# Kernel optimization log

Measured on AMD Instinct MI355X. Metric: run time of the kernel, lower is better.

Reference implementation:

```python
import jax, jax.numpy as jnp
import numpy as np

EPS = 1e-5  # BatchNorm1d default eps

def _conv1d(x, w, stride, pad):
    # x: [B, Cin, L], w: [Cout, Cin, K]
    return jax.lax.conv_general_dilated(
        x, w, window_strides=(stride,), padding=[(pad, pad)],
        dimension_numbers=('NCH', 'OIH', 'NCH'))

def _bn(x, g, b, m, v):
    # eval-mode BatchNorm1d with running stats; x: [B, C, L]
    scale = g / jnp.sqrt(v + EPS)
    return x * scale[None, :, None] + (b - m * scale)[None, :, None]

def _hardtanh(x):
    return jnp.clip(x, -1.0, 1.0)

def _maxpool2(x):
    B, C, L = x.shape
    return x.reshape(B, C, L // 2, 2).max(axis=-1)


def setup_inputs() -> dict:
    key = jax.random.key(0)
    ks = jax.random.split(key, 20)
    B, L = 256, 16384
    x = jax.random.normal(ks[0], (B, 1, L), dtype=jnp.float32)
    rms = jax.random.uniform(ks[1], (B, 1), dtype=jnp.float32)
    # conv weights (fan-in scaled)
    w1 = jax.random.normal(ks[2], (16, 1, 17), dtype=jnp.float32) * (1.0 / np.sqrt(1 * 17))
    w2 = jax.random.normal(ks[3], (32, 16, 9), dtype=jnp.float32) * (1.0 / np.sqrt(16 * 9))
    w3 = jax.random.normal(ks[4], (64, 32, 5), dtype=jnp.float32) * (1.0 / np.sqrt(32 * 5))
    # batchnorm params (eval mode: gamma, beta, running mean/var)
    def bn_params(k, C):
        k1, k2, k3, k4 = jax.random.split(k, 4)
        g = 1.0 + 0.1 * jax.random.normal(k1, (C,), dtype=jnp.float32)
        b = 0.1 * jax.random.normal(k2, (C,), dtype=jnp.float32)
        m = 0.1 * jax.random.normal(k3, (C,), dtype=jnp.float32)
        v = jax.random.uniform(k4, (C,), dtype=jnp.float32, minval=0.5, maxval=1.5)
        return g, b, m, v
    g1, b1, m1, v1 = bn_params(ks[5], 16)
    g2, b2, m2, v2 = bn_params(ks[6], 32)
    g3, b3, m3, v3 = bn_params(ks[7], 64)
    fc1_w = jax.random.normal(ks[8], (32, 65), dtype=jnp.float32) * (1.0 / np.sqrt(65))
    fc1_b = jnp.zeros((32,), dtype=jnp.float32)
    fc2_w = jax.random.normal(ks[9], (2, 32), dtype=jnp.float32) * (1.0 / np.sqrt(32))
    fc2_b = jnp.zeros((2,), dtype=jnp.float32)
    return dict(x=x, rms=rms, w1=w1, g1=g1, b1=b1, m1=m1, v1=v1,
                w2=w2, g2=g2, b2=b2, m2=m2, v2=v2,
                w3=w3, g3=g3, b3=b3, m3=m3, v3=v3,
                fc1_w=fc1_w, fc1_b=fc1_b, fc2_w=fc2_w, fc2_b=fc2_b)


def reference(x, rms, w1, g1, b1, m1, v1, w2, g2, b2, m2, v2,
              w3, g3, b3, m3, v3, fc1_w, fc1_b, fc2_w, fc2_b):
    # Stage 1: float conv
    h = _conv1d(x, w1, 2, 8)                 # [B,16,8192]
    h = _maxpool2(_hardtanh(_bn(h, g1, b1, m1, v1)))  # [B,16,4096]
    # Stage 2: binarized (sign) weight conv
    h = _conv1d(h, jnp.sign(w2), 2, 4)       # [B,32,2048]
    h = _maxpool2(_hardtanh(_bn(h, g2, b2, m2, v2)))  # [B,32,1024]
    # Stage 3: binarized weight conv
    h = _conv1d(h, jnp.sign(w3), 2, 2)       # [B,64,512]
    h = _maxpool2(_hardtanh(_bn(h, g3, b3, m3, v3)))  # [B,64,256]
    feat = h.mean(axis=-1)                   # AdaptiveAvgPool1d(1) -> [B,64]
    combined = jnp.concatenate([feat, rms], axis=1)   # [B,65]
    h = _hardtanh(combined @ fc1_w.T + fc1_b)
    return h @ fc2_w.T + fc2_b               # [B,2]
```

## Files before the change

### kernel.cpp

```cpp
#include <hip/hip_runtime.h>

#define EPS 1e-5f

typedef float f32x4 __attribute__((ext_vector_type(4)));
typedef short s16x8 __attribute__((ext_vector_type(8)));

union FragU { uint4 u; s16x8 s; };

__device__ __forceinline__ float ht(float x){ return fminf(fmaxf(x,-1.f),1.f); }
__device__ __forceinline__ float sgn(float v){ return (v>0.f)?1.f:((v<0.f)?-1.f:0.f); }
__device__ __forceinline__ unsigned short f2bf(float f){
    unsigned int u = __builtin_bit_cast(unsigned int, f);
    u += 0x7FFFu + ((u>>16)&1u);
    return (unsigned short)(u>>16);
}

__global__ __launch_bounds__(512) void prep(
    const float* __restrict__ w1, const float* __restrict__ w2, const float* __restrict__ w3,
    const float* g1,const float* b1,const float* m1,const float* v1,
    const float* g2,const float* b2,const float* m2,const float* v2,
    const float* g3,const float* b3,const float* m3,const float* v3,
    unsigned short* __restrict__ a1, unsigned short* __restrict__ a2,
    unsigned short* __restrict__ a3, float* __restrict__ bn){
  const int t = threadIdx.x;
  if(t < 64){
    int q = t>>4, m = t&15;
    #pragma unroll
    for(int j=0;j<8;++j){ int k = 8*q+j;
      a1[t*8+j] = f2bf((k<17)? w1[m*17+k] : 0.f); }
  }
  for(int e = t; e < 640; e += 512){
    int m = e&15, q = (e>>4)&3, hc = e>>6, c = hc%5, h = hc/5;
    int oc = m + 16*h, k = 2*c + (q>>1);
    #pragma unroll
    for(int j=0;j<8;++j){ int ic = 8*(q&1)+j;
      a2[e*8+j] = f2bf((k<9)? sgn(w2[(oc*16+ic)*9+k]) : 0.f); }
  }
  for(int e = t; e < 1280; e += 512){
    int m = e&15, q = (e>>4)&3, gc = e>>6, c = gc%5, g = gc/5;
    int oc = m + 16*g;
    #pragma unroll
    for(int j=0;j<8;++j){ int ic = 8*q+j;
      a3[e*8+j] = f2bf(sgn(w3[(oc*32+ic)*5+c])); }
  }
  if(t<16){ float s = g1[t]*rsqrtf(v1[t]+EPS); bn[t]    = s; bn[16+t]  = b1[t]-m1[t]*s; }
  if(t<32){ float s = g2[t]*rsqrtf(v2[t]+EPS); bn[32+t] = s; bn[64+t]  = b2[t]-m2[t]*s; }
  if(t<64){ float s = g3[t]*rsqrtf(v3[t]+EPS); bn[96+t] = s; bn[160+t] = b3[t]-m3[t]*s; }
}

__global__ __launch_bounds__(512, 4) void kfused(const float* __restrict__ x,
    const unsigned short* __restrict__ a1, const unsigned short* __restrict__ a2,
    const unsigned short* __restrict__ a3, const float* __restrict__ bn,
    float* __restrict__ partial){
  __shared__ __align__(16) unsigned short xs[2176];
  __shared__ __align__(16) unsigned short s1[552*24];
  __shared__ __align__(16) unsigned short s2[132*40];
  __shared__ float fws[8*32];
  const int b  = blockIdx.x >> 3;
  const int t  = blockIdx.x & 7;
  const int Q0 = 32*t;
  const int tid = threadIdx.x;
  const int lane = tid & 63, m = lane & 15, q = lane >> 4, w = tid >> 6;

  const int x0 = 64*Q0 - 56;
  const float* xrow = &x[b*16384];
  for(int i = tid; i < 544; i += 512){
    int g0 = x0 + 4*i;
    float4 v = make_float4(0.f,0.f,0.f,0.f);
    if(g0 >= 0 && g0 <= 16380) v = *(const float4*)&xrow[g0];
    uint2 pk;
    pk.x = (unsigned)f2bf(v.x) | ((unsigned)f2bf(v.y)<<16);
    pk.y = (unsigned)f2bf(v.z) | ((unsigned)f2bf(v.w)<<16);
    *(uint2*)&xs[4*i] = pk;
  }
  FragU af1; af1.u = *(const uint4*)&a1[(q*16+m)*8];
  const float4 sc1 = *(const float4*)&bn[4*q];
  const float4 sh1 = *(const float4*)&bn[16+4*q];
  __syncthreads();

  const unsigned* X32 = (const unsigned*)xs;
  for(int it = 0; it < 9; ++it){
    int tile = it*8 + w;
    if(tile < 67){
      int nl = tile*16 + m;
      int d = nl + 4*q;
      FragU bf;
      bf.u.x = X32[d]; bf.u.y = X32[d+1]; bf.u.z = X32[d+2]; bf.u.w = X32[d+3];
      f32x4 acc = {0.f,0.f,0.f,0.f};
      acc = __builtin_amdgcn_mfma_f32_16x16x32_bf16(af1.s, bf.s, acc, 0,0,0);
      float r0 = ht(acc[0]*sc1.x + sh1.x);
      float r1 = ht(acc[1]*sc1.y + sh1.y);
      float r2 = ht(acc[2]*sc1.z + sh1.z);
      float r3 = ht(acc[3]*sc1.w + sh1.w);
      float p0 = fmaxf(r0, __shfl_xor(r0,1,64));
      float p1 = fmaxf(r1, __shfl_xor(r1,1,64));
      float p2 = fmaxf(r2, __shfl_xor(r2,1,64));
      float p3 = fmaxf(r3, __shfl_xor(r3,1,64));
      if((m&1)==0){
        int ppl = nl >> 1;
        uint2 pk;
        pk.x = (unsigned)f2bf(p0) | ((unsigned)f2bf(p1)<<16);
        pk.y = (unsigned)f2bf(p2) | ((unsigned)f2bf(p3)<<16);
        *(uint2*)&s1[ppl*24 + 4*q] = pk;
      }
    }
  }
  __syncthreads();

  FragU af2[2][5];
  #pragma unroll
  for(int h=0;h<2;++h)
    #pragma unroll
    for(int c=0;c<5;++c)
      af2[h][c].u = *(const uint4*)&a2[(((h*5+c)*4+q)*16+m)*8];
  float4 sc2[2], sh2[2];
  #pragma unroll
  for(int h=0;h<2;++h){
    sc2[h] = *(const float4*)&bn[32 + 16*h + 4*q];
    sh2[h] = *(const float4*)&bn[64 + 16*h + 4*q];
  }
  for(int it = 0; it < 3; ++it){
    int tile = it*8 + w;
    if(tile < 17){
      int nl = tile*16 + m;
      f32x4 acc[2] = {{0.f,0.f,0.f,0.f},{0.f,0.f,0.f,0.f}};
      #pragma unroll
      for(int c=0;c<5;++c){
        int row = 2*nl + 2*c + (q>>1);
        FragU bf; bf.u = *(const uint4*)&s1[row*24 + 8*(q&1)];
        acc[0] = __builtin_amdgcn_mfma_f32_16x16x32_bf16(af2[0][c].s, bf.s, acc[0],0,0,0);
        acc[1] = __builtin_amdgcn_mfma_f32_16x16x32_bf16(af2[1][c].s, bf.s, acc[1],0,0,0);
      }
      #pragma unroll
      for(int h=0;h<2;++h){
        float r0 = ht(acc[h][0]*sc2[h].x + sh2[h].x);
        float r1 = ht(acc[h][1]*sc2[h].y + sh2[h].y);
        float r2 = ht(acc[h][2]*sc2[h].z + sh2[h].z);
        float r3 = ht(acc[h][3]*sc2[h].w + sh2[h].w);
        float p0 = fmaxf(r0, __shfl_xor(r0,1,64));
        float p1 = fmaxf(r1, __shfl_xor(r1,1,64));
        float p2 = fmaxf(r2, __shfl_xor(r2,1,64));
        float p3 = fmaxf(r3, __shfl_xor(r3,1,64));
        if((m&1)==0 && nl < 264){
          int ppl = nl >> 1;
          uint2 pk;
          pk.x = (unsigned)f2bf(p0) | ((unsigned)f2bf(p1)<<16);
          pk.y = (unsigned)f2bf(p2) | ((unsigned)f2bf(p3)<<16);
          *(uint2*)&s2[ppl*40 + 16*h + 4*q] = pk;
        }
      }
    }
  }
  __syncthreads();

  const int gw = w >> 2, tw = w & 3;
  FragU af3[2][5];
  #pragma unroll
  for(int gl=0;gl<2;++gl)
    #pragma unroll
    for(int c=0;c<5;++c)
      af3[gl][c].u = *(const uint4*)&a3[((((2*gw+gl)*5+c)*4+q)*16+m)*8];
  float4 sc3[2], sh3[2];
  #pragma unroll
  for(int gl=0;gl<2;++gl){
    sc3[gl] = *(const float4*)&bn[96  + 16*(2*gw+gl) + 4*q];
    sh3[gl] = *(const float4*)&bn[160 + 16*(2*gw+gl) + 4*q];
  }
  {
    int nl = tw*16 + m;
    f32x4 acc[2] = {{0.f,0.f,0.f,0.f},{0.f,0.f,0.f,0.f}};
    #pragma unroll
    for(int c=0;c<5;++c){
      int row = 2*nl + c;
      FragU bf; bf.u = *(const uint4*)&s2[row*40 + 8*q];
      acc[0] = __builtin_amdgcn_mfma_f32_16x16x32_bf16(af3[0][c].s, bf.s, acc[0],0,0,0);
      acc[1] = __builtin_amdgcn_mfma_f32_16x16x32_bf16(af3[1][c].s, bf.s, acc[1],0,0,0);
    }
    #pragma unroll
    for(int gl=0;gl<2;++gl){
      float r0 = ht(acc[gl][0]*sc3[gl].x + sh3[gl].x);
      float r1 = ht(acc[gl][1]*sc3[gl].y + sh3[gl].y);
      float r2 = ht(acc[gl][2]*sc3[gl].z + sh3[gl].z);
      float r3 = ht(acc[gl][3]*sc3[gl].w + sh3[gl].w);
      float p0 = fmaxf(r0, __shfl_xor(r0,1,64));
      float p1 = fmaxf(r1, __shfl_xor(r1,1,64));
      float p2 = fmaxf(r2, __shfl_xor(r2,1,64));
      float p3 = fmaxf(r3, __shfl_xor(r3,1,64));
      float s0 = p0, s1v = p1, s2v = p2, s3 = p3;
      s0 += __shfl_xor(s0,2,64); s0 += __shfl_xor(s0,4,64); s0 += __shfl_xor(s0,8,64);
      s1v += __shfl_xor(s1v,2,64); s1v += __shfl_xor(s1v,4,64); s1v += __shfl_xor(s1v,8,64);
      s2v += __shfl_xor(s2v,2,64); s2v += __shfl_xor(s2v,4,64); s2v += __shfl_xor(s2v,8,64);
      s3 += __shfl_xor(s3,2,64); s3 += __shfl_xor(s3,4,64); s3 += __shfl_xor(s3,8,64);
      if(m == 0)
        *(float4*)&fws[w*32 + 16*gl + 4*q] = make_float4(s0,s1v,s2v,s3);
    }
  }
  __syncthreads();
  if(tid < 64){
    int oc = tid;
    int wb = (oc >> 5) * 4;
    int ocl = oc & 31;
    float sum = fws[wb*32+ocl] + fws[(wb+1)*32+ocl] + fws[(wb+2)*32+ocl] + fws[(wb+3)*32+ocl];
    partial[(b*8 + t)*64 + oc] = sum;
  }
}

__global__ __launch_bounds__(64) void kfc(const float* __restrict__ partial,
    const float* __restrict__ rms, const float* __restrict__ fc1w,
    const float* __restrict__ fc1b, const float* __restrict__ fc2w,
    const float* __restrict__ fc2b, float* __restrict__ out){
  __shared__ float feat[64];
  __shared__ float hbuf[32];
  const int b = blockIdx.x, tid = threadIdx.x;
  float s = 0.f;
  #pragma unroll
  for(int t = 0; t < 8; ++t) s += partial[(b*8 + t)*64 + tid];
  feat[tid] = s * (1.f/256.f);
  __syncthreads();
  if(tid < 32){
    float acc = fc1b[tid];
    const float* wv = &fc1w[tid*65];
    #pragma unroll
    for(int c = 0; c < 64; ++c) acc += wv[c]*feat[c];
    acc += wv[64]*rms[b];
    hbuf[tid] = ht(acc);
  }
  __syncthreads();
  if(tid < 2){
    float acc = fc2b[tid];
    const float* wv = &fc2w[tid*32];
    #pragma unroll
    for(int j = 0; j < 32; ++j) acc += wv[j]*hbuf[j];
    out[b*2 + tid] = acc;
  }
}

extern "C" void kernel_launch(void* const* d_in, const int* in_sizes, int n_in,
                              void* d_out, int out_size, void* d_ws, size_t ws_size,
                              hipStream_t stream){
  (void)in_sizes; (void)n_in; (void)out_size; (void)ws_size;
  const float* x    = (const float*)d_in[0];
  const float* rms  = (const float*)d_in[1];
  const float* w1   = (const float*)d_in[2];
  const float* g1   = (const float*)d_in[3];
  const float* b1   = (const float*)d_in[4];
  const float* m1   = (const float*)d_in[5];
  const float* v1   = (const float*)d_in[6];
  const float* w2   = (const float*)d_in[7];
  const float* g2   = (const float*)d_in[8];
  const float* b2   = (const float*)d_in[9];
  const float* m2   = (const float*)d_in[10];
  const float* v2   = (const float*)d_in[11];
  const float* w3   = (const float*)d_in[12];
  const float* g3   = (const float*)d_in[13];
  const float* b3   = (const float*)d_in[14];
  const float* m3   = (const float*)d_in[15];
  const float* v3   = (const float*)d_in[16];
  const float* fc1w = (const float*)d_in[17];
  const float* fc1b = (const float*)d_in[18];
  const float* fc2w = (const float*)d_in[19];
  const float* fc2b = (const float*)d_in[20];
  float* out  = (float*)d_out;

  float*          partial = (float*)d_ws;
  unsigned short* a1  = (unsigned short*)(partial + 131072);
  unsigned short* a2  = a1 + 512;
  unsigned short* a3  = a2 + 5120;
  float*          bnp = (float*)(a3 + 10240);

  prep<<<1,    512, 0, stream>>>(w1, w2, w3, g1,b1,m1,v1, g2,b2,m2,v2, g3,b3,m3,v3,
                                 a1, a2, a3, bnp);
  kfused<<<2048, 512, 0, stream>>>(x, a1, a2, a3, bnp, partial);
  kfc<<<256, 64, 0, stream>>>(partial, rms, fc1w, fc1b, fc2w, fc2b, out);
}
```

Before: 141.3 us.

## Fuse FC head into conv kernel via last-block counter and use DPP reductions

The separate FC-head kernel is removed. Each of the 8 tiles per batch row now bumps an atomic counter, and the last one to finish sums the partials and computes fc1/fc2 in place, which saves a kernel launch. The lane shuffles for max-pool and the 16-lane sum now use DPP moves instead of __shfl_xor, cutting LDS permute traffic. The row sum runs over all 16 lanes and is halved to make up for the duplicated pairs. The prep kernel is split across 7 blocks and also zeroes the counters, at the cost of an extra threadfence and atomic per block.

```diff
diff --git a/kernel.cpp b/kernel.cpp
--- a/kernel.cpp
+++ b/kernel.cpp
@@ -15,52 +15,83 @@
     return (unsigned short)(u>>16);
 }
 
+#define DPP_XOR1 0xB1
+#define DPP_ROR1 0x121
+#define DPP_ROR2 0x122
+#define DPP_ROR4 0x124
+#define DPP_ROR8 0x128
+template<int C>
+__device__ __forceinline__ float dppf(float x){
+  return __builtin_bit_cast(float, __builtin_amdgcn_update_dpp(
+      0, __builtin_bit_cast(int, x), C, 0xF, 0xF, true));
+}
+__device__ __forceinline__ float poolmax(float r){ return fmaxf(r, dppf<DPP_XOR1>(r)); }
+__device__ __forceinline__ float rowsum16(float s){
+  s += dppf<DPP_ROR8>(s); s += dppf<DPP_ROR4>(s);
+  s += dppf<DPP_ROR2>(s); s += dppf<DPP_ROR1>(s);
+  return s;
+}
+
 __global__ __launch_bounds__(512) void prep(
     const float* __restrict__ w1, const float* __restrict__ w2, const float* __restrict__ w3,
     const float* g1,const float* b1,const float* m1,const float* v1,
     const float* g2,const float* b2,const float* m2,const float* v2,
     const float* g3,const float* b3,const float* m3,const float* v3,
     unsigned short* __restrict__ a1, unsigned short* __restrict__ a2,
-    unsigned short* __restrict__ a3, float* __restrict__ bn){
-  const int t = threadIdx.x;
-  if(t < 64){
-    int q = t>>4, m = t&15;
-    #pragma unroll
-    for(int j=0;j<8;++j){ int k = 8*q+j;
-      a1[t*8+j] = f2bf((k<17)? w1[m*17+k] : 0.f); }
-  }
-  for(int e = t; e < 640; e += 512){
-    int m = e&15, q = (e>>4)&3, hc = e>>6, c = hc%5, h = hc/5;
-    int oc = m + 16*h, k = 2*c + (q>>1);
-    #pragma unroll
-    for(int j=0;j<8;++j){ int ic = 8*(q&1)+j;
-      a2[e*8+j] = f2bf((k<9)? sgn(w2[(oc*16+ic)*9+k]) : 0.f); }
-  }
-  for(int e = t; e < 1280; e += 512){
-    int m = e&15, q = (e>>4)&3, gc = e>>6, c = gc%5, g = gc/5;
-    int oc = m + 16*g;
-    #pragma unroll
-    for(int j=0;j<8;++j){ int ic = 8*q+j;
-      a3[e*8+j] = f2bf(sgn(w3[(oc*32+ic)*5+c])); }
-  }
-  if(t<16){ float s = g1[t]*rsqrtf(v1[t]+EPS); bn[t]    = s; bn[16+t]  = b1[t]-m1[t]*s; }
-  if(t<32){ float s = g2[t]*rsqrtf(v2[t]+EPS); bn[32+t] = s; bn[64+t]  = b2[t]-m2[t]*s; }
-  if(t<64){ float s = g3[t]*rsqrtf(v3[t]+EPS); bn[96+t] = s; bn[160+t] = b3[t]-m3[t]*s; }
+    unsigned short* __restrict__ a3, float* __restrict__ bn, int* __restrict__ cnt){
+  const int t = threadIdx.x, bid = blockIdx.x;
+  if(bid == 0){
+    if(t < 64){
+      int q = t>>4, m = t&15;
+      #pragma unroll
+      for(int j=0;j<8;++j){ int k = 8*q+j;
+        a1[t*8+j] = f2bf((k<17)? w1[m*17+k] : 0.f); }
+    }
+    if(t<16){ float s = g1[t]*rsqrtf(v1[t]+EPS); bn[t]    = s; bn[16+t]  = b1[t]-m1[t]*s; }
+    if(t<32){ float s = g2[t]*rsqrtf(v2[t]+EPS); bn[32+t] = s; bn[64+t]  = b2[t]-m2[t]*s; }
+    if(t<64){ float s = g3[t]*rsqrtf(v3[t]+EPS); bn[96+t] = s; bn[160+t] = b3[t]-m3[t]*s; }
+  } else if(bid <= 2){
+    int e = (bid-1)*512 + t;
+    if(e < 640){
+      int m = e&15, q = (e>>4)&3, hc = e>>6, c = hc%5, h = hc/5;
+      int oc = m + 16*h, k = 2*c + (q>>1);
+      #pragma unroll
+      for(int j=0;j<8;++j){ int ic = 8*(q&1)+j;
+        a2[e*8+j] = f2bf((k<9)? sgn(w2[(oc*16+ic)*9+k]) : 0.f); }
+    }
+  } else if(bid <= 5){
+    int e = (bid-3)*512 + t;
+    if(e < 1280){
+      int m = e&15, q = (e>>4)&3, gc = e>>6, c = gc%5, g = gc/5;
+      int oc = m + 16*g;
+      #pragma unroll
+      for(int j=0;j<8;++j){ int ic = 8*q+j;
+        a3[e*8+j] = f2bf(sgn(w3[(oc*32+ic)*5+c])); }
+    }
+  } else {
+    if(t < 256) cnt[t] = 0;
+  }
 }
 
 __global__ __launch_bounds__(512, 4) void kfused(const float* __restrict__ x,
     const unsigned short* __restrict__ a1, const unsigned short* __restrict__ a2,
     const unsigned short* __restrict__ a3, const float* __restrict__ bn,
-    float* __restrict__ partial){
+    float* __restrict__ partial, int* __restrict__ cnt,
+    const float* __restrict__ rms, const float* __restrict__ fc1w,
+    const float* __restrict__ fc1b, const float* __restrict__ fc2w,
+    const float* __restrict__ fc2b, float* __restrict__ out){
   __shared__ __align__(16) unsigned short xs[2176];
   __shared__ __align__(16) unsigned short s1[552*24];
   __shared__ __align__(16) unsigned short s2[132*40];
   __shared__ float fws[8*32];
+  __shared__ float feat[64];
+  __shared__ float hbuf[32];
+  __shared__ int   lastFlag;
   const int b  = blockIdx.x >> 3;
   const int t  = blockIdx.x & 7;
   const int Q0 = 32*t;
   const int tid = threadIdx.x;
-  const int lane = tid & 63, m = lane & 15, q = lane >> 4, w = tid >> 6;
+  const int m = tid & 15, q = (tid & 63) >> 4, w = tid >> 6;
 
   const int x0 = 64*Q0 - 56;
   const float* xrow = &x[b*16384];
@@ -88,14 +119,10 @@
       bf.u.x = X32[d]; bf.u.y = X32[d+1]; bf.u.z = X32[d+2]; bf.u.w = X32[d+3];
       f32x4 acc = {0.f,0.f,0.f,0.f};
       acc = __builtin_amdgcn_mfma_f32_16x16x32_bf16(af1.s, bf.s, acc, 0,0,0);
-      float r0 = ht(acc[0]*sc1.x + sh1.x);
-      float r1 = ht(acc[1]*sc1.y + sh1.y);
-      float r2 = ht(acc[2]*sc1.z + sh1.z);
-      float r3 = ht(acc[3]*sc1.w + sh1.w);
-      float p0 = fmaxf(r0, __shfl_xor(r0,1,64));
-      float p1 = fmaxf(r1, __shfl_xor(r1,1,64));
-      float p2 = fmaxf(r2, __shfl_xor(r2,1,64));
-      float p3 = fmaxf(r3, __shfl_xor(r3,1,64));
+      float p0 = poolmax(ht(acc[0]*sc1.x + sh1.x));
+      float p1 = poolmax(ht(acc[1]*sc1.y + sh1.y));
+      float p2 = poolmax(ht(acc[2]*sc1.z + sh1.z));
+      float p3 = poolmax(ht(acc[3]*sc1.w + sh1.w));
       if((m&1)==0){
         int ppl = nl >> 1;
         uint2 pk;
@@ -133,14 +160,10 @@
       }
       #pragma unroll
       for(int h=0;h<2;++h){
-        float r0 = ht(acc[h][0]*sc2[h].x + sh2[h].x);
-        float r1 = ht(acc[h][1]*sc2[h].y + sh2[h].y);
-        float r2 = ht(acc[h][2]*sc2[h].z + sh2[h].z);
-        float r3 = ht(acc[h][3]*sc2[h].w + sh2[h].w);
-        float p0 = fmaxf(r0, __shfl_xor(r0,1,64));
-        float p1 = fmaxf(r1, __shfl_xor(r1,1,64));
-        float p2 = fmaxf(r2, __shfl_xor(r2,1,64));
-        float p3 = fmaxf(r3, __shfl_xor(r3,1,64));
+        float p0 = poolmax(ht(acc[h][0]*sc2[h].x + sh2[h].x));
+        float p1 = poolmax(ht(acc[h][1]*sc2[h].y + sh2[h].y));
+        float p2 = poolmax(ht(acc[h][2]*sc2[h].z + sh2[h].z));
+        float p3 = poolmax(ht(acc[h][3]*sc2[h].w + sh2[h].w));
         if((m&1)==0 && nl < 264){
           int ppl = nl >> 1;
           uint2 pk;
@@ -178,60 +201,54 @@
     }
     #pragma unroll
     for(int gl=0;gl<2;++gl){
-      float r0 = ht(acc[gl][0]*sc3[gl].x + sh3[gl].x);
-      float r1 = ht(acc[gl][1]*sc3[gl].y + sh3[gl].y);
-      float r2 = ht(acc[gl][2]*sc3[gl].z + sh3[gl].z);
-      float r3 = ht(acc[gl][3]*sc3[gl].w + sh3[gl].w);
-      float p0 = fmaxf(r0, __shfl_xor(r0,1,64));
-      float p1 = fmaxf(r1, __shfl_xor(r1,1,64));
-      float p2 = fmaxf(r2, __shfl_xor(r2,1,64));
-      float p3 = fmaxf(r3, __shfl_xor(r3,1,64));
-      float s0 = p0, s1v = p1, s2v = p2, s3 = p3;
-      s0 += __shfl_xor(s0,2,64); s0 += __shfl_xor(s0,4,64); s0 += __shfl_xor(s0,8,64);
-      s1v += __shfl_xor(s1v,2,64); s1v += __shfl_xor(s1v,4,64); s1v += __shfl_xor(s1v,8,64);
-      s2v += __shfl_xor(s2v,2,64); s2v += __shfl_xor(s2v,4,64); s2v += __shfl_xor(s2v,8,64);
-      s3 += __shfl_xor(s3,2,64); s3 += __shfl_xor(s3,4,64); s3 += __shfl_xor(s3,8,64);
+      float p0 = poolmax(ht(acc[gl][0]*sc3[gl].x + sh3[gl].x));
+      float p1 = poolmax(ht(acc[gl][1]*sc3[gl].y + sh3[gl].y));
+      float p2 = poolmax(ht(acc[gl][2]*sc3[gl].z + sh3[gl].z));
+      float p3 = poolmax(ht(acc[gl][3]*sc3[gl].w + sh3[gl].w));
+      float s0 = rowsum16(p0)*0.5f, s1v = rowsum16(p1)*0.5f;
+      float s2v = rowsum16(p2)*0.5f, s3 = rowsum16(p3)*0.5f;
       if(m == 0)
         *(float4*)&fws[w*32 + 16*gl + 4*q] = make_float4(s0,s1v,s2v,s3);
     }
   }
   __syncthreads();
   if(tid < 64){
-    int oc = tid;
-    int wb = (oc >> 5) * 4;
-    int ocl = oc & 31;
+    int ocl = tid & 31;
+    int wb  = (tid >> 5) * 4;
     float sum = fws[wb*32+ocl] + fws[(wb+1)*32+ocl] + fws[(wb+2)*32+ocl] + fws[(wb+3)*32+ocl];
-    partial[(b*8 + t)*64 + oc] = sum;
-  }
-}
-
-__global__ __launch_bounds__(64) void kfc(const float* __restrict__ partial,
-    const float* __restrict__ rms, const float* __restrict__ fc1w,
-    const float* __restrict__ fc1b, const float* __restrict__ fc2w,
-    const float* __restrict__ fc2b, float* __restrict__ out){
-  __shared__ float feat[64];
-  __shared__ float hbuf[32];
-  const int b = blockIdx.x, tid = threadIdx.x;
-  float s = 0.f;
-  #pragma unroll
-  for(int t = 0; t < 8; ++t) s += partial[(b*8 + t)*64 + tid];
-  feat[tid] = s * (1.f/256.f);
-  __syncthreads();
-  if(tid < 32){
-    float acc = fc1b[tid];
-    const float* wv = &fc1w[tid*65];
-    #pragma unroll
-    for(int c = 0; c < 64; ++c) acc += wv[c]*feat[c];
-    acc += wv[64]*rms[b];
-    hbuf[tid] = ht(acc);
-  }
-  __syncthreads();
-  if(tid < 2){
-    float acc = fc2b[tid];
-    const float* wv = &fc2w[tid*32];
-    #pragma unroll
-    for(int j = 0; j < 32; ++j) acc += wv[j]*hbuf[j];
-    out[b*2 + tid] = acc;
+    partial[(b*8 + t)*64 + tid] = sum;
+  }
+  if(tid == 0){
+    __threadfence();
+    int old = atomicAdd(&cnt[b], 1);
+    lastFlag = (old == 7);
+  }
+  __syncthreads();
+  if(lastFlag){
+    if(tid < 64){
+      const volatile float* pv = partial;
+      float s = 0.f;
+      #pragma unroll
+      for(int t2 = 0; t2 < 8; ++t2) s += pv[(b*8 + t2)*64 + tid];
+      feat[tid] = s * (1.f/256.f);
+    }
+    __syncthreads();
+    if(tid < 32){
+      float acc = fc1b[tid];
+      const float* wv = &fc1w[tid*65];
+      #pragma unroll
+      for(int c = 0; c < 64; ++c) acc += wv[c]*feat[c];
+      acc += wv[64]*rms[b];
+      hbuf[tid] = ht(acc);
+    }
+    __syncthreads();
+    if(tid < 2){
+      float acc = fc2b[tid];
+      const float* wv = &fc2w[tid*32];
+      #pragma unroll
+      for(int j = 0; j < 32; ++j) acc += wv[j]*hbuf[j];
+      out[b*2 + tid] = acc;
+    }
   }
 }
 
@@ -267,9 +284,10 @@
   unsigned short* a2  = a1 + 512;
   unsigned short* a3  = a2 + 5120;
   float*          bnp = (float*)(a3 + 10240);
-
-  prep<<<1,    512, 0, stream>>>(w1, w2, w3, g1,b1,m1,v1, g2,b2,m2,v2, g3,b3,m3,v3,
-                                 a1, a2, a3, bnp);
-  kfused<<<2048, 512, 0, stream>>>(x, a1, a2, a3, bnp, partial);
-  kfc<<<256, 64, 0, stream>>>(partial, rms, fc1w, fc1b, fc2w, fc2b, out);
-}
+  int*            cnt = (int*)(bnp + 224);
+
+  prep<<<7,    512, 0, stream>>>(w1, w2, w3, g1,b1,m1,v1, g2,b2,m2,v2, g3,b3,m3,v3,
+                                 a1, a2, a3, bnp, cnt);
+  kfused<<<2048, 512, 0, stream>>>(x, a1, a2, a3, bnp, partial, cnt,
+                                   rms, fc1w, fc1b, fc2w, fc2b, out);
+}
```

Measured after the change: 163.2 us. 1.15x slower.

## Halve per-block sequence tile, raise occupancy, and parallelize weight prep

Applied to the files above, without the earlier changes.

Each fused block now covers 16 pooled stage-3 outputs instead of 32. This doubles the grid to 4096 blocks, shrinks the LDS buffers, and raises launch_bounds occupancy to 8 blocks per CU. Stage-3 work is redistributed so each wave handles one 16-channel group, and halo positions outside the valid range are explicitly zeroed. The prep kernel is split across 6 blocks so weight packing runs in parallel. In exchange, the halo overhead ratio rises, since more redundant stage-1/2 work is recomputed per output, and there are twice as many partial sums to reduce.

```diff
diff --git a/kernel.cpp b/kernel.cpp
--- a/kernel.cpp
+++ b/kernel.cpp
@@ -22,49 +22,55 @@
     const float* g3,const float* b3,const float* m3,const float* v3,
     unsigned short* __restrict__ a1, unsigned short* __restrict__ a2,
     unsigned short* __restrict__ a3, float* __restrict__ bn){
-  const int t = threadIdx.x;
-  if(t < 64){
-    int q = t>>4, m = t&15;
-    #pragma unroll
-    for(int j=0;j<8;++j){ int k = 8*q+j;
-      a1[t*8+j] = f2bf((k<17)? w1[m*17+k] : 0.f); }
-  }
-  for(int e = t; e < 640; e += 512){
-    int m = e&15, q = (e>>4)&3, hc = e>>6, c = hc%5, h = hc/5;
-    int oc = m + 16*h, k = 2*c + (q>>1);
-    #pragma unroll
-    for(int j=0;j<8;++j){ int ic = 8*(q&1)+j;
-      a2[e*8+j] = f2bf((k<9)? sgn(w2[(oc*16+ic)*9+k]) : 0.f); }
-  }
-  for(int e = t; e < 1280; e += 512){
-    int m = e&15, q = (e>>4)&3, gc = e>>6, c = gc%5, g = gc/5;
-    int oc = m + 16*g;
-    #pragma unroll
-    for(int j=0;j<8;++j){ int ic = 8*q+j;
-      a3[e*8+j] = f2bf(sgn(w3[(oc*32+ic)*5+c])); }
-  }
-  if(t<16){ float s = g1[t]*rsqrtf(v1[t]+EPS); bn[t]    = s; bn[16+t]  = b1[t]-m1[t]*s; }
-  if(t<32){ float s = g2[t]*rsqrtf(v2[t]+EPS); bn[32+t] = s; bn[64+t]  = b2[t]-m2[t]*s; }
-  if(t<64){ float s = g3[t]*rsqrtf(v3[t]+EPS); bn[96+t] = s; bn[160+t] = b3[t]-m3[t]*s; }
-}
-
-__global__ __launch_bounds__(512, 4) void kfused(const float* __restrict__ x,
+  const int t = threadIdx.x, bid = blockIdx.x;
+  if(bid == 0){
+    if(t < 64){
+      int q = t>>4, m = t&15;
+      #pragma unroll
+      for(int j=0;j<8;++j){ int k = 8*q+j;
+        a1[t*8+j] = f2bf((k<17)? w1[m*17+k] : 0.f); }
+    }
+    if(t<16){ float s = g1[t]*rsqrtf(v1[t]+EPS); bn[t]    = s; bn[16+t]  = b1[t]-m1[t]*s; }
+    if(t<32){ float s = g2[t]*rsqrtf(v2[t]+EPS); bn[32+t] = s; bn[64+t]  = b2[t]-m2[t]*s; }
+    if(t<64){ float s = g3[t]*rsqrtf(v3[t]+EPS); bn[96+t] = s; bn[160+t] = b3[t]-m3[t]*s; }
+  } else if(bid <= 2){
+    int e = (bid-1)*512 + t;
+    if(e < 640){
+      int m = e&15, q = (e>>4)&3, hc = e>>6, c = hc%5, h = hc/5;
+      int oc = m + 16*h, k = 2*c + (q>>1);
+      #pragma unroll
+      for(int j=0;j<8;++j){ int ic = 8*(q&1)+j;
+        a2[e*8+j] = f2bf((k<9)? sgn(w2[(oc*16+ic)*9+k]) : 0.f); }
+    }
+  } else {
+    int e = (bid-3)*512 + t;
+    if(e < 1280){
+      int m = e&15, q = (e>>4)&3, gc = e>>6, c = gc%5, g = gc/5;
+      int oc = m + 16*g;
+      #pragma unroll
+      for(int j=0;j<8;++j){ int ic = 8*q+j;
+        a3[e*8+j] = f2bf(sgn(w3[(oc*32+ic)*5+c])); }
+    }
+  }
+}
+
+__global__ __launch_bounds__(512, 8) void kfused(const float* __restrict__ x,
     const unsigned short* __restrict__ a1, const unsigned short* __restrict__ a2,
     const unsigned short* __restrict__ a3, const float* __restrict__ bn,
     float* __restrict__ partial){
-  __shared__ __align__(16) unsigned short xs[2176];
-  __shared__ __align__(16) unsigned short s1[552*24];
-  __shared__ __align__(16) unsigned short s2[132*40];
-  __shared__ float fws[8*32];
-  const int b  = blockIdx.x >> 3;
-  const int t  = blockIdx.x & 7;
-  const int Q0 = 32*t;
+  __shared__ __align__(16) unsigned short xs[1160];
+  __shared__ __align__(16) unsigned short s1[296*24];
+  __shared__ __align__(16) unsigned short s2[68*40];
+  __shared__ float fws[8*16];
+  const int b  = blockIdx.x >> 4;
+  const int t  = blockIdx.x & 15;
+  const int Q0 = 16*t;
   const int tid = threadIdx.x;
-  const int lane = tid & 63, m = lane & 15, q = lane >> 4, w = tid >> 6;
+  const int m = tid & 15, q = (tid & 63) >> 4, w = tid >> 6;
 
   const int x0 = 64*Q0 - 56;
   const float* xrow = &x[b*16384];
-  for(int i = tid; i < 544; i += 512){
+  for(int i = tid; i < 288; i += 512){
     int g0 = x0 + 4*i;
     float4 v = make_float4(0.f,0.f,0.f,0.f);
     if(g0 >= 0 && g0 <= 16380) v = *(const float4*)&xrow[g0];
@@ -79,9 +85,9 @@
   __syncthreads();
 
   const unsigned* X32 = (const unsigned*)xs;
-  for(int it = 0; it < 9; ++it){
+  for(int it = 0; it < 5; ++it){
     int tile = it*8 + w;
-    if(tile < 67){
+    if(tile < 35){
       int nl = tile*16 + m;
       int d = nl + 4*q;
       FragU bf;
@@ -98,9 +104,10 @@
       float p3 = fmaxf(r3, __shfl_xor(r3,1,64));
       if((m&1)==0){
         int ppl = nl >> 1;
+        bool ok = (unsigned)(16*Q0 - 12 + ppl) < 4096u;
         uint2 pk;
-        pk.x = (unsigned)f2bf(p0) | ((unsigned)f2bf(p1)<<16);
-        pk.y = (unsigned)f2bf(p2) | ((unsigned)f2bf(p3)<<16);
+        pk.x = ok ? ((unsigned)f2bf(p0) | ((unsigned)f2bf(p1)<<16)) : 0u;
+        pk.y = ok ? ((unsigned)f2bf(p2) | ((unsigned)f2bf(p3)<<16)) : 0u;
         *(uint2*)&s1[ppl*24 + 4*q] = pk;
       }
     }
@@ -119,9 +126,9 @@
     sc2[h] = *(const float4*)&bn[32 + 16*h + 4*q];
     sh2[h] = *(const float4*)&bn[64 + 16*h + 4*q];
   }
-  for(int it = 0; it < 3; ++it){
+  for(int it = 0; it < 2; ++it){
     int tile = it*8 + w;
-    if(tile < 17){
+    if(tile < 9){
       int nl = tile*16 + m;
       f32x4 acc[2] = {{0.f,0.f,0.f,0.f},{0.f,0.f,0.f,0.f}};
       #pragma unroll
@@ -141,11 +148,12 @@
         float p1 = fmaxf(r1, __shfl_xor(r1,1,64));
         float p2 = fmaxf(r2, __shfl_xor(r2,1,64));
         float p3 = fmaxf(r3, __shfl_xor(r3,1,64));
-        if((m&1)==0 && nl < 264){
+        if((m&1)==0 && nl < 136){
           int ppl = nl >> 1;
+          bool ok = (unsigned)(4*Q0 - 2 + ppl) < 1024u;
           uint2 pk;
-          pk.x = (unsigned)f2bf(p0) | ((unsigned)f2bf(p1)<<16);
-          pk.y = (unsigned)f2bf(p2) | ((unsigned)f2bf(p3)<<16);
+          pk.x = ok ? ((unsigned)f2bf(p0) | ((unsigned)f2bf(p1)<<16)) : 0u;
+          pk.y = ok ? ((unsigned)f2bf(p2) | ((unsigned)f2bf(p3)<<16)) : 0u;
           *(uint2*)&s2[ppl*40 + 16*h + 4*q] = pk;
         }
       }
@@ -153,55 +161,42 @@
   }
   __syncthreads();
 
-  const int gw = w >> 2, tw = w & 3;
-  FragU af3[2][5];
-  #pragma unroll
-  for(int gl=0;gl<2;++gl)
-    #pragma unroll
-    for(int c=0;c<5;++c)
-      af3[gl][c].u = *(const uint4*)&a3[((((2*gw+gl)*5+c)*4+q)*16+m)*8];
-  float4 sc3[2], sh3[2];
-  #pragma unroll
-  for(int gl=0;gl<2;++gl){
-    sc3[gl] = *(const float4*)&bn[96  + 16*(2*gw+gl) + 4*q];
-    sh3[gl] = *(const float4*)&bn[160 + 16*(2*gw+gl) + 4*q];
-  }
+  const int og = w >> 1, tw = w & 1;
+  FragU af3[5];
+  #pragma unroll
+  for(int c=0;c<5;++c)
+    af3[c].u = *(const uint4*)&a3[(((og*5+c)*4+q)*16+m)*8];
+  const float4 sc3 = *(const float4*)&bn[96  + 16*og + 4*q];
+  const float4 sh3 = *(const float4*)&bn[160 + 16*og + 4*q];
   {
     int nl = tw*16 + m;
-    f32x4 acc[2] = {{0.f,0.f,0.f,0.f},{0.f,0.f,0.f,0.f}};
+    f32x4 acc = {0.f,0.f,0.f,0.f};
     #pragma unroll
     for(int c=0;c<5;++c){
       int row = 2*nl + c;
       FragU bf; bf.u = *(const uint4*)&s2[row*40 + 8*q];
-      acc[0] = __builtin_amdgcn_mfma_f32_16x16x32_bf16(af3[0][c].s, bf.s, acc[0],0,0,0);
-      acc[1] = __builtin_amdgcn_mfma_f32_16x16x32_bf16(af3[1][c].s, bf.s, acc[1],0,0,0);
-    }
-    #pragma unroll
-    for(int gl=0;gl<2;++gl){
-      float r0 = ht(acc[gl][0]*sc3[gl].x + sh3[gl].x);
-      float r1 = ht(acc[gl][1]*sc3[gl].y + sh3[gl].y);
-      float r2 = ht(acc[gl][2]*sc3[gl].z + sh3[gl].z);
-      float r3 = ht(acc[gl][3]*sc3[gl].w + sh3[gl].w);
-      float p0 = fmaxf(r0, __shfl_xor(r0,1,64));
-      float p1 = fmaxf(r1, __shfl_xor(r1,1,64));
-      float p2 = fmaxf(r2, __shfl_xor(r2,1,64));
-      float p3 = fmaxf(r3, __shfl_xor(r3,1,64));
-      float s0 = p0, s1v = p1, s2v = p2, s3 = p3;
-      s0 += __shfl_xor(s0,2,64); s0 += __shfl_xor(s0,4,64); s0 += __shfl_xor(s0,8,64);
-      s1v += __shfl_xor(s1v,2,64); s1v += __shfl_xor(s1v,4,64); s1v += __shfl_xor(s1v,8,64);
-      s2v += __shfl_xor(s2v,2,64); s2v += __shfl_xor(s2v,4,64); s2v += __shfl_xor(s2v,8,64);
-      s3 += __shfl_xor(s3,2,64); s3 += __shfl_xor(s3,4,64); s3 += __shfl_xor(s3,8,64);
-      if(m == 0)
-        *(float4*)&fws[w*32 + 16*gl + 4*q] = make_float4(s0,s1v,s2v,s3);
-    }
+      acc = __builtin_amdgcn_mfma_f32_16x16x32_bf16(af3[c].s, bf.s, acc, 0,0,0);
+    }
+    float r0 = ht(acc[0]*sc3.x + sh3.x);
+    float r1 = ht(acc[1]*sc3.y + sh3.y);
+    float r2 = ht(acc[2]*sc3.z + sh3.z);
+    float r3 = ht(acc[3]*sc3.w + sh3.w);
+    float p0 = fmaxf(r0, __shfl_xor(r0,1,64));
+    float p1 = fmaxf(r1, __shfl_xor(r1,1,64));
+    float p2 = fmaxf(r2, __shfl_xor(r2,1,64));
+    float p3 = fmaxf(r3, __shfl_xor(r3,1,64));
+    p0 += __shfl_xor(p0,2,64); p0 += __shfl_xor(p0,4,64); p0 += __shfl_xor(p0,8,64);
+    p1 += __shfl_xor(p1,2,64); p1 += __shfl_xor(p1,4,64); p1 += __shfl_xor(p1,8,64);
+    p2 += __shfl_xor(p2,2,64); p2 += __shfl_xor(p2,4,64); p2 += __shfl_xor(p2,8,64);
+    p3 += __shfl_xor(p3,2,64); p3 += __shfl_xor(p3,4,64); p3 += __shfl_xor(p3,8,64);
+    if(m == 0)
+      *(float4*)&fws[w*16 + 4*q] = make_float4(p0,p1,p2,p3);
   }
   __syncthreads();
   if(tid < 64){
-    int oc = tid;
-    int wb = (oc >> 5) * 4;
-    int ocl = oc & 31;
-    float sum = fws[wb*32+ocl] + fws[(wb+1)*32+ocl] + fws[(wb+2)*32+ocl] + fws[(wb+3)*32+ocl];
-    partial[(b*8 + t)*64 + oc] = sum;
+    int og2 = tid >> 4, ocl = tid & 15;
+    float sum = fws[(2*og2)*16 + ocl] + fws[(2*og2+1)*16 + ocl];
+    partial[(b*16 + t)*64 + tid] = sum;
   }
 }
 
@@ -214,7 +209,7 @@
   const int b = blockIdx.x, tid = threadIdx.x;
   float s = 0.f;
   #pragma unroll
-  for(int t = 0; t < 8; ++t) s += partial[(b*8 + t)*64 + tid];
+  for(int t = 0; t < 16; ++t) s += partial[(b*16 + t)*64 + tid];
   feat[tid] = s * (1.f/256.f);
   __syncthreads();
   if(tid < 32){
@@ -263,13 +258,13 @@
   float* out  = (float*)d_out;
 
   float*          partial = (float*)d_ws;
-  unsigned short* a1  = (unsigned short*)(partial + 131072);
+  unsigned short* a1  = (unsigned short*)(partial + 262144);
   unsigned short* a2  = a1 + 512;
   unsigned short* a3  = a2 + 5120;
   float*          bnp = (float*)(a3 + 10240);
 
-  prep<<<1,    512, 0, stream>>>(w1, w2, w3, g1,b1,m1,v1, g2,b2,m2,v2, g3,b3,m3,v3,
+  prep<<<6,    512, 0, stream>>>(w1, w2, w3, g1,b1,m1,v1, g2,b2,m2,v2, g3,b3,m3,v3,
                                  a1, a2, a3, bnp);
-  kfused<<<2048, 512, 0, stream>>>(x, a1, a2, a3, bnp, partial);
+  kfused<<<4096, 512, 0, stream>>>(x, a1, a2, a3, bnp, partial);
   kfc<<<256, 64, 0, stream>>>(partial, rms, fc1w, fc1b, fc2w, fc2b, out);
 }
```

Result: slower. 198.1 us (+40.2%).
